# Optimization experiments

Hardware: AMD Instinct MI355X
Metric: run time of the kernel (lower is better)

## Reference

```python
import jax, jax.numpy as jnp
import numpy as np

LN_EPS = 1e-12
BIG = 1e30
BAND = 15  # end index may be at most 15 tokens after start


def output_layer(x, w1, b1, g, b, w2, b2):
    # Linear -> ReLU -> LayerNorm -> Linear (dropout is identity at eval)
    h = jax.nn.relu(x @ w1 + b1)
    mu = jnp.mean(h, axis=-1, keepdims=True)
    var = jnp.mean(jnp.square(h - mu), axis=-1, keepdims=True)
    h = (h - mu) * jax.lax.rsqrt(var + LN_EPS) * g + b
    return h @ w2 + b2


def setup_inputs() -> dict:
    key = jax.random.key(0)
    ks = jax.random.split(key, 8)
    B, S, D = 8, 4096, 1024
    H2 = 2 * D
    inp = {
        "context_input": jax.random.normal(ks[0], (B, S, D), jnp.float32),
        "context_mask": jnp.ones((B, S), jnp.float32),
    }
    def head(k1, k2, n_ans):
        return (
            0.02 * jax.random.normal(k1, (D, H2), jnp.float32),
            jnp.zeros((H2,), jnp.float32),
            jnp.ones((H2,), jnp.float32),
            jnp.zeros((H2,), jnp.float32),
            0.02 * jax.random.normal(k2, (H2, n_ans), jnp.float32),
            jnp.zeros((n_ans,), jnp.float32),
        )
    for name, k1, k2, n_ans in [("start", ks[1], ks[2], 1), ("end", ks[3], ks[4], 1), ("type", ks[5], ks[6], 4)]:
        w1, b1, g, b, w2, b2 = head(k1, k2, n_ans)
        inp[f"{name}_w1"] = w1; inp[f"{name}_b1"] = b1
        inp[f"{name}_g"] = g; inp[f"{name}_b"] = b
        inp[f"{name}_w2"] = w2; inp[f"{name}_b2"] = b2
    return inp


def reference(context_input, context_mask,
              start_w1, start_b1, start_g, start_b, start_w2, start_b2,
              end_w1, end_b1, end_g, end_b, end_w2, end_b2,
              type_w1, type_b1, type_g, type_b, type_w2, type_b2):
    S = context_input.shape[1]
    start_pred = output_layer(context_input, start_w1, start_b1, start_g, start_b, start_w2, start_b2)[..., 0] \
        - BIG * (1.0 - context_mask)  # [B,S]
    end_pred = output_layer(context_input, end_w1, end_b1, end_g, end_b, end_w2, end_b2)[..., 0] \
        - BIG * (1.0 - context_mask)  # [B,S]
    type_pred = output_layer(context_input[:, 0, :], type_w1, type_b1, type_g, type_b, type_w2, type_b2)  # [B,4]

    # outer[b,i,j] = start[b,i] + end[b,j], masked to band 0 <= j-i <= 15
    outer = start_pred[:, :, None] + end_pred[:, None, :]  # [B,S,S]
    i = jnp.arange(S)[:, None]
    j = jnp.arange(S)[None, :]
    band = ((j >= i) & (j <= i + BAND)).astype(outer.dtype)  # [S,S]
    outer = outer - BIG * (1.0 - band)[None]

    yp1 = jnp.argmax(jnp.max(outer, axis=2), axis=1)  # best start index [B]
    yp2 = jnp.argmax(jnp.max(outer, axis=1), axis=1)  # best end index [B]
    return start_pred, end_pred, type_pred, yp1, yp2
```

## Files before the change

kernel.cpp:

```cpp
#include <hip/hip_runtime.h>

typedef _Float16 f16x8 __attribute__((ext_vector_type(8)));
typedef float f32x4 __attribute__((ext_vector_type(4)));

#define BIGF 1e30f
#define M_TOT 32768
#define H2 2048

#define WS_XH 0u
#define WS_WT 67108864u
#define WS_BVEC 75497472u
#define WS_GW2 75513856u
#define WS_CONSTS 75530240u
#define WS_PART 75530496u
#define WS_TPART 100696320u

__global__ void k_convert_x(const float* __restrict__ x, _Float16* __restrict__ xh) {
  size_t i = ((size_t)blockIdx.x * 256 + threadIdx.x) * 8;
  float4 v0 = *(const float4*)(x + i);
  float4 v1 = *(const float4*)(x + i + 4);
  f16x8 h;
  h[0] = (_Float16)v0.x; h[1] = (_Float16)v0.y; h[2] = (_Float16)v0.z; h[3] = (_Float16)v0.w;
  h[4] = (_Float16)v1.x; h[5] = (_Float16)v1.y; h[6] = (_Float16)v1.z; h[7] = (_Float16)v1.w;
  *(f16x8*)(xh + i) = h;
}

__global__ void k_convert_w(const float* __restrict__ w_s, const float* __restrict__ w_e,
                            _Float16* __restrict__ wt) {
  __shared__ float tile[64][65];
  const float* w = blockIdx.z ? w_e : w_s;
  int n0 = blockIdx.x * 64, k0 = blockIdx.y * 64;
  int tx = threadIdx.x & 63, ty = threadIdx.x >> 6;
#pragma unroll
  for (int i = ty; i < 64; i += 4) tile[i][tx] = w[(size_t)(k0 + i) * H2 + n0 + tx];
  __syncthreads();
#pragma unroll
  for (int i = ty; i < 64; i += 4) {
    wt[((size_t)(blockIdx.z * H2 + n0 + i)) * 1024 + k0 + tx] = (_Float16)tile[tx][i];
  }
}

__global__ void k_prep(const float* __restrict__ s_b1, const float* __restrict__ s_g,
                       const float* __restrict__ s_w2, const float* __restrict__ s_b,
                       const float* __restrict__ s_b2, const float* __restrict__ e_b1,
                       const float* __restrict__ e_g, const float* __restrict__ e_w2,
                       const float* __restrict__ e_b, const float* __restrict__ e_b2,
                       float* __restrict__ bvec, float* __restrict__ gw2,
                       float* __restrict__ consts) {
  int blk = blockIdx.x;
  if (blk < 16) {
    int i = blk * 256 + threadIdx.x;
    int head = i >> 11, j = i & (H2 - 1);
    bvec[i] = head ? e_b1[j] : s_b1[j];
    gw2[i] = head ? e_g[j] * e_w2[j] : s_g[j] * s_w2[j];
  } else {
    int h = blk - 16;
    const float* g = h ? e_g : s_g;
    const float* b = h ? e_b : s_b;
    const float* w2 = h ? e_w2 : s_w2;
    const float* b2 = h ? e_b2 : s_b2;
    float c1 = 0.f, c2 = 0.f;
    for (int j = threadIdx.x; j < H2; j += 256) {
      float w = w2[j];
      c1 += g[j] * w;
      c2 += b[j] * w;
    }
    for (int m = 1; m < 64; m <<= 1) { c1 += __shfl_xor(c1, m); c2 += __shfl_xor(c2, m); }
    __shared__ float r1[4], r2[4];
    int wid = threadIdx.x >> 6;
    if ((threadIdx.x & 63) == 0) { r1[wid] = c1; r2[wid] = c2; }
    __syncthreads();
    if (threadIdx.x == 0) {
      consts[h * 2 + 0] = r1[0] + r1[1] + r1[2] + r1[3];
      consts[h * 2 + 1] = r2[0] + r2[1] + r2[2] + r2[3] + b2[0];
    }
  }
}

#define BUF 65536u
#define STA(q, tile, bufo)                                                              \
  __builtin_amdgcn_global_load_lds(                                                     \
      (const __attribute__((address_space(1))) unsigned int*)(srcA + (size_t)(q) * 131072 + (size_t)(tile) * 128), \
      (__attribute__((address_space(3))) unsigned int*)(lds + (bufo) + (q) * 8192 + t * 16), 16, 0, 0)
#define STB(q, tile, bufo)                                                              \
  __builtin_amdgcn_global_load_lds(                                                     \
      (const __attribute__((address_space(1))) unsigned int*)(srcB + (size_t)(q) * 131072 + (size_t)(tile) * 128), \
      (__attribute__((address_space(3))) unsigned int*)(lds + (bufo) + 32768u + (q) * 8192 + t * 16), 16, 0, 0)

#define READA(AF, mi0, BUFO)                                                            \
  AF[0][0] = *(const f16x8*)(lds + (BUFO) + arow + (mi0) * 2048 + low0);                \
  AF[0][1] = *(const f16x8*)(lds + (BUFO) + arow + (mi0) * 2048 + low1);                \
  AF[1][0] = *(const f16x8*)(lds + (BUFO) + arow + ((mi0) + 1) * 2048 + low0);          \
  AF[1][1] = *(const f16x8*)(lds + (BUFO) + arow + ((mi0) + 1) * 2048 + low1);

#define READB(BF, BUFO)                                                                 \
  _Pragma("unroll")                                                                     \
  for (int nj = 0; nj < 4; ++nj) {                                                      \
    BF[nj][0] = *(const f16x8*)(lds + (BUFO) + brow + nj * 2048 + low0);                \
    BF[nj][1] = *(const f16x8*)(lds + (BUFO) + brow + nj * 2048 + low1);                \
  }

#define MFMA2(m0, m1, AF, BF)                                                           \
  __builtin_amdgcn_s_setprio(1);                                                        \
  _Pragma("unroll")                                                                     \
  for (int nj = 0; nj < 4; ++nj) {                                                      \
    acc[m0][nj] = __builtin_amdgcn_mfma_f32_16x16x32_f16(AF[0][0], BF[nj][0], acc[m0][nj], 0, 0, 0); \
    acc[m1][nj] = __builtin_amdgcn_mfma_f32_16x16x32_f16(AF[1][0], BF[nj][0], acc[m1][nj], 0, 0, 0); \
  }                                                                                     \
  _Pragma("unroll")                                                                     \
  for (int nj = 0; nj < 4; ++nj) {                                                      \
    acc[m0][nj] = __builtin_amdgcn_mfma_f32_16x16x32_f16(AF[0][1], BF[nj][1], acc[m0][nj], 0, 0, 0); \
    acc[m1][nj] = __builtin_amdgcn_mfma_f32_16x16x32_f16(AF[1][1], BF[nj][1], acc[m1][nj], 0, 0, 0); \
  }                                                                                     \
  __builtin_amdgcn_s_setprio(0);

#define PHASE_TAIL                                                                      \
  __builtin_amdgcn_sched_barrier(0);                                                    \
  __builtin_amdgcn_s_barrier();                                                         \
  asm volatile("s_waitcnt lgkmcnt(0)" ::: "memory");                                    \
  __builtin_amdgcn_sched_barrier(0);

__global__ __launch_bounds__(512, 2) void k_gemm(const _Float16* __restrict__ Xh,
                                                 const _Float16* __restrict__ Wt,
                                                 const float* __restrict__ bvec,
                                                 const float* __restrict__ gw2,
                                                 float* __restrict__ partials) {
  __shared__ char lds[2 * BUF];
  const int bid = blockIdx.x;
  const int swzb = (bid & 7) * 256 + (bid >> 3);
  const int nb = swzb & 15;
  const int mb = swzb >> 4;
  const int t = threadIdx.x;
  const int lane = t & 63, wid = t >> 6;
  const int c15 = lane & 15, g4 = lane >> 4;
  const int wmg = wid >> 2;
  const int wn = (wid & 3) * 64;

  f32x4 acc[8][4];
#pragma unroll
  for (int i = 0; i < 8; ++i)
#pragma unroll
    for (int j = 0; j < 4; ++j) acc[i][j] = (f32x4){0.f, 0.f, 0.f, 0.f};

  const char* Abase = (const char*)(Xh + (size_t)mb * 256 * 1024);
  const char* Bbase = (const char*)(Wt + (size_t)nb * 256 * 1024);
  const int rowl = t >> 3;
  const int swz = ((t & 7) * 16) ^ ((rowl & 7) << 4);
  const char* srcA = Abase + (size_t)rowl * 2048 + swz;
  const char* srcB = Bbase + (size_t)rowl * 2048 + swz;

  const int xorv = (c15 & 7) << 4;
  const int low0 = (g4 * 16) ^ xorv;
  const int low1 = (64 + g4 * 16) ^ xorv;
  const int arow = (wmg * 128 + c15) * 128;
  const int brow = 32768 + (wn + c15) * 128;

  STA(0, 0, 0); STA(1, 0, 0); STA(2, 0, 0); STA(3, 0, 0);
  STB(0, 0, 0); STB(1, 0, 0); STB(2, 0, 0); STB(3, 0, 0);
  STB(0, 1, BUF); STB(1, 1, BUF); STB(2, 1, BUF); STB(3, 1, BUF);
  STA(0, 1, BUF); STA(2, 1, BUF);
  asm volatile("s_waitcnt vmcnt(6)" ::: "memory");
  __builtin_amdgcn_s_barrier();
  __builtin_amdgcn_sched_barrier(0);

  f16x8 af[2][2], bf[4][2];

#pragma unroll
  for (int g = 0; g < 16; ++g) {
    const unsigned OB = (unsigned)(g & 1) * BUF;
    const unsigned ON = OB ^ BUF;
    READB(bf, OB);
    READA(af, 0, OB);
    if (g < 15) { STA(1, g + 1, ON); STA(3, g + 1, ON); }
    PHASE_TAIL
    MFMA2(0, 1, af, bf);
    READA(af, 2, OB);
    if (g < 14) { STB(0, g + 2, OB); STB(1, g + 2, OB); }
    PHASE_TAIL
    MFMA2(2, 3, af, bf);
    READA(af, 4, OB);
    if (g < 14) { STB(2, g + 2, OB); STB(3, g + 2, OB); }
    PHASE_TAIL
    MFMA2(4, 5, af, bf);
    READA(af, 6, OB);
    if (g < 14) { STA(0, g + 2, OB); STA(2, g + 2, OB); }
    PHASE_TAIL
    MFMA2(6, 7, af, bf);
    if (g < 14) asm volatile("s_waitcnt vmcnt(6)" ::: "memory");
    else        asm volatile("s_waitcnt vmcnt(0)" ::: "memory");
    __builtin_amdgcn_s_barrier();
  }

  float bv[4], gv[4];
#pragma unroll
  for (int nj = 0; nj < 4; ++nj) {
    int col = nb * 256 + wn + nj * 16 + c15;
    bv[nj] = bvec[col];
    gv[nj] = gw2[col];
  }
  const int slice = nb * 4 + (wid & 3);
#pragma unroll
  for (int mi = 0; mi < 8; ++mi) {
#pragma unroll
    for (int r = 0; r < 4; ++r) {
      float s1 = 0.f, s2 = 0.f, s3 = 0.f;
#pragma unroll
      for (int nj = 0; nj < 4; ++nj) {
        float v = acc[mi][nj][r] + bv[nj];
        v = fmaxf(v, 0.f);
        s1 += v;
        s2 += v * v;
        s3 += v * gv[nj];
      }
#pragma unroll
      for (int m = 1; m < 16; m <<= 1) {
        s1 += __shfl_xor(s1, m);
        s2 += __shfl_xor(s2, m);
        s3 += __shfl_xor(s3, m);
      }
      if (c15 == 0) {
        int rowg = mb * 256 + wmg * 128 + mi * 16 + g4 * 4 + r;
        partials[((size_t)(slice * 3 + 0)) * M_TOT + rowg] = s1;
        partials[((size_t)(slice * 3 + 1)) * M_TOT + rowg] = s2;
        partials[((size_t)(slice * 3 + 2)) * M_TOT + rowg] = s3;
      }
    }
  }
}

__global__ void k_reduce(const float* __restrict__ partials, const float* __restrict__ consts,
                         const float* __restrict__ mask, float* __restrict__ out) {
  int m = blockIdx.x * 256 + threadIdx.x;
  float s1 = 0.f, s2 = 0.f, s3 = 0.f, e1 = 0.f, e2 = 0.f, e3 = 0.f;
  for (int nb2 = 0; nb2 < 32; ++nb2) {
    s1 += partials[((size_t)(nb2 * 3 + 0)) * M_TOT + m];
    s2 += partials[((size_t)(nb2 * 3 + 1)) * M_TOT + m];
    s3 += partials[((size_t)(nb2 * 3 + 2)) * M_TOT + m];
  }
  for (int nb2 = 32; nb2 < 64; ++nb2) {
    e1 += partials[((size_t)(nb2 * 3 + 0)) * M_TOT + m];
    e2 += partials[((size_t)(nb2 * 3 + 1)) * M_TOT + m];
    e3 += partials[((size_t)(nb2 * 3 + 2)) * M_TOT + m];
  }
  const float H = (float)H2;
  float mu = s1 / H;
  float var = fmaxf(s2 / H - mu * mu, 0.f);
  float rs = 1.f / sqrtf(var + 1e-12f);
  float score_s = rs * (s3 - mu * consts[0]) + consts[1];
  mu = e1 / H;
  var = fmaxf(e2 / H - mu * mu, 0.f);
  rs = 1.f / sqrtf(var + 1e-12f);
  float score_e = rs * (e3 - mu * consts[2]) + consts[3];
  float mk = BIGF * (1.f - mask[m]);
  out[m] = score_s - mk;
  out[M_TOT + m] = score_e - mk;
}

__global__ void k_type_partial(const float* __restrict__ X, const float* __restrict__ w1,
                               const float* __restrict__ b1, const float* __restrict__ g,
                               const float* __restrict__ w2, float* __restrict__ tpart) {
  __shared__ float xs[1024];
  int cb = blockIdx.x, tok = blockIdx.y, t = threadIdx.x;
  const float* xp = X + (size_t)tok * 4096 * 1024;
  for (int i = t; i < 1024; i += 256) xs[i] = xp[i];
  __syncthreads();
  int j = cb * 256 + t;
  float dot = 0.f;
  for (int k = 0; k < 1024; ++k) dot += xs[k] * w1[(size_t)k * H2 + j];
  float h = fmaxf(dot + b1[j], 0.f);
  float gj = g[j];
  float s[6];
  s[0] = h;
  s[1] = h * h;
#pragma unroll
  for (int c = 0; c < 4; ++c) s[2 + c] = h * gj * w2[j * 4 + c];
  for (int m = 1; m < 64; m <<= 1)
#pragma unroll
    for (int q = 0; q < 6; ++q) s[q] += __shfl_xor(s[q], m);
  __shared__ float red[4][6];
  int wid = t >> 6;
  if ((t & 63) == 0)
#pragma unroll
    for (int q = 0; q < 6; ++q) red[wid][q] = s[q];
  __syncthreads();
  if (t == 0)
#pragma unroll
    for (int q = 0; q < 6; ++q)
      tpart[(tok * 8 + cb) * 6 + q] = red[0][q] + red[1][q] + red[2][q] + red[3][q];
}

__global__ void k_type_final(const float* __restrict__ tpart, const float* __restrict__ g,
                             const float* __restrict__ bb, const float* __restrict__ w2,
                             const float* __restrict__ b2, float* __restrict__ out) {
  int t = threadIdx.x;
  float c1[4] = {0.f, 0.f, 0.f, 0.f}, c2[4] = {0.f, 0.f, 0.f, 0.f};
  for (int j = t; j < H2; j += 256) {
    float gj = g[j], bj = bb[j];
#pragma unroll
    for (int c = 0; c < 4; ++c) {
      float w = w2[j * 4 + c];
      c1[c] += gj * w;
      c2[c] += bj * w;
    }
  }
  for (int m = 1; m < 64; m <<= 1)
#pragma unroll
    for (int c = 0; c < 4; ++c) { c1[c] += __shfl_xor(c1[c], m); c2[c] += __shfl_xor(c2[c], m); }
  __shared__ float rC1[4][4], rC2[4][4];
  int wid = t >> 6;
  if ((t & 63) == 0)
#pragma unroll
    for (int c = 0; c < 4; ++c) { rC1[wid][c] = c1[c]; rC2[wid][c] = c2[c]; }
  __syncthreads();
  __shared__ float sC1[4], sC2[4];
  if (t < 4) {
    sC1[t] = rC1[0][t] + rC1[1][t] + rC1[2][t] + rC1[3][t];
    sC2[t] = rC2[0][t] + rC2[1][t] + rC2[2][t] + rC2[3][t];
  }
  __syncthreads();
  if (t < 32) {
    int tok = t >> 2, c = t & 3;
    float s1 = 0.f, s2 = 0.f, s3 = 0.f;
    for (int cb = 0; cb < 8; ++cb) {
      s1 += tpart[(tok * 8 + cb) * 6 + 0];
      s2 += tpart[(tok * 8 + cb) * 6 + 1];
      s3 += tpart[(tok * 8 + cb) * 6 + 2 + c];
    }
    float mu = s1 / (float)H2;
    float var = fmaxf(s2 / (float)H2 - mu * mu, 0.f);
    float rs = 1.f / sqrtf(var + 1e-12f);
    out[65536 + tok * 4 + c] = rs * (s3 - mu * sC1[c]) + sC2[c] + b2[c];
  }
}

__global__ void k_band(const float* __restrict__ preds, float* __restrict__ out) {
  __shared__ float ss[4096], se[4096];
  int b = blockIdx.x, t = threadIdx.x;
  for (int i = t; i < 4096; i += 256) {
    ss[i] = preds[(size_t)b * 4096 + i];
    se[i] = preds[M_TOT + (size_t)b * 4096 + i];
  }
  __syncthreads();
  float bv1 = -3.0e38f, bv2 = -3.0e38f;
  int bi1 = 0x7fffffff, bi2 = 0x7fffffff;
  for (int i = t; i < 4096; i += 256) {
    float m1 = -3.0e38f;
    int jmax = i + 15 < 4095 ? i + 15 : 4095;
    for (int j = i; j <= jmax; ++j) m1 = fmaxf(m1, se[j]);
    float v1 = ss[i] + m1;
    if (v1 > bv1 || (v1 == bv1 && i < bi1)) { bv1 = v1; bi1 = i; }
    float m2 = -3.0e38f;
    int imin = i - 15 > 0 ? i - 15 : 0;
    for (int j = imin; j <= i; ++j) m2 = fmaxf(m2, ss[j]);
    float v2 = se[i] + m2;
    if (v2 > bv2 || (v2 == bv2 && i < bi2)) { bv2 = v2; bi2 = i; }
  }
  for (int m = 1; m < 64; m <<= 1) {
    float ov = __shfl_xor(bv1, m);
    int oi = __shfl_xor(bi1, m);
    if (ov > bv1 || (ov == bv1 && oi < bi1)) { bv1 = ov; bi1 = oi; }
    ov = __shfl_xor(bv2, m);
    oi = __shfl_xor(bi2, m);
    if (ov > bv2 || (ov == bv2 && oi < bi2)) { bv2 = ov; bi2 = oi; }
  }
  __shared__ float rv[2][4];
  __shared__ int ri[2][4];
  int wid = t >> 6;
  if ((t & 63) == 0) { rv[0][wid] = bv1; ri[0][wid] = bi1; rv[1][wid] = bv2; ri[1][wid] = bi2; }
  __syncthreads();
  if (t == 0) {
    float v = rv[0][0];
    int ix = ri[0][0];
    for (int w = 1; w < 4; ++w)
      if (rv[0][w] > v || (rv[0][w] == v && ri[0][w] < ix)) { v = rv[0][w]; ix = ri[0][w]; }
    out[65568 + b] = (float)ix;
    v = rv[1][0];
    ix = ri[1][0];
    for (int w = 1; w < 4; ++w)
      if (rv[1][w] > v || (rv[1][w] == v && ri[1][w] < ix)) { v = rv[1][w]; ix = ri[1][w]; }
    out[65576 + b] = (float)ix;
  }
}

extern "C" void kernel_launch(void* const* d_in, const int* in_sizes, int n_in, void* d_out,
                              int out_size, void* d_ws, size_t ws_size, hipStream_t stream) {
  const float* X = (const float*)d_in[0];
  const float* mask = (const float*)d_in[1];
  const float* s_w1 = (const float*)d_in[2];
  const float* s_b1 = (const float*)d_in[3];
  const float* s_g = (const float*)d_in[4];
  const float* s_b = (const float*)d_in[5];
  const float* s_w2 = (const float*)d_in[6];
  const float* s_b2 = (const float*)d_in[7];
  const float* e_w1 = (const float*)d_in[8];
  const float* e_b1 = (const float*)d_in[9];
  const float* e_g = (const float*)d_in[10];
  const float* e_b = (const float*)d_in[11];
  const float* e_w2 = (const float*)d_in[12];
  const float* e_b2 = (const float*)d_in[13];
  const float* t_w1 = (const float*)d_in[14];
  const float* t_b1 = (const float*)d_in[15];
  const float* t_g = (const float*)d_in[16];
  const float* t_b = (const float*)d_in[17];
  const float* t_w2 = (const float*)d_in[18];
  const float* t_b2 = (const float*)d_in[19];

  char* ws = (char*)d_ws;
  _Float16* Xh = (_Float16*)(ws + WS_XH);
  _Float16* Wt = (_Float16*)(ws + WS_WT);
  float* bvec = (float*)(ws + WS_BVEC);
  float* gw2 = (float*)(ws + WS_GW2);
  float* consts = (float*)(ws + WS_CONSTS);
  float* partials = (float*)(ws + WS_PART);
  float* tpart = (float*)(ws + WS_TPART);
  float* out = (float*)d_out;

  k_convert_x<<<16384, 256, 0, stream>>>(X, Xh);
  k_convert_w<<<dim3(32, 16, 2), 256, 0, stream>>>(s_w1, e_w1, Wt);
  k_prep<<<18, 256, 0, stream>>>(s_b1, s_g, s_w2, s_b, s_b2, e_b1, e_g, e_w2, e_b, e_b2,
                                 bvec, gw2, consts);
  k_gemm<<<2048, 512, 0, stream>>>(Xh, Wt, bvec, gw2, partials);
  k_reduce<<<128, 256, 0, stream>>>(partials, consts, mask, out);
  k_type_partial<<<dim3(8, 8), 256, 0, stream>>>(X, t_w1, t_b1, t_g, t_w2, tpart);
  k_type_final<<<1, 256, 0, stream>>>(tpart, t_g, t_b, t_w2, t_b2, out);
  k_band<<<8, 256, 0, stream>>>(out, out);
}
```

Baseline: 422.9 us.

## Load B fragments directly from global into registers, stage only A in LDS

The GEMM kernel stops staging the weight (B) tile through LDS. Each lane now loads its B fragments straight from global memory into double-buffered registers one k-step ahead, and only the activation (A) tile goes through LDS via global_load_lds. This halves LDS usage and removes the B LDS reads and the per-phase barriers. The costs are uncoalesced per-lane 16-byte global loads for B, more registers, and a full vmcnt(0) wait each k-iteration, which leaves less overlap between loads and compute.

```diff
diff --git a/kernel.cpp b/kernel.cpp
--- a/kernel.cpp
+++ b/kernel.cpp
@@ -77,55 +77,58 @@
   }
 }
 
-#define BUF 65536u
-#define STA(q, tile, bufo)                                                              \
-  __builtin_amdgcn_global_load_lds(                                                     \
-      (const __attribute__((address_space(1))) unsigned int*)(srcA + (size_t)(q) * 131072 + (size_t)(tile) * 128), \
-      (__attribute__((address_space(3))) unsigned int*)(lds + (bufo) + (q) * 8192 + t * 16), 16, 0, 0)
-#define STB(q, tile, bufo)                                                              \
-  __builtin_amdgcn_global_load_lds(                                                     \
-      (const __attribute__((address_space(1))) unsigned int*)(srcB + (size_t)(q) * 131072 + (size_t)(tile) * 128), \
-      (__attribute__((address_space(3))) unsigned int*)(lds + (bufo) + 32768u + (q) * 8192 + t * 16), 16, 0, 0)
-
-#define READA(AF, mi0, BUFO)                                                            \
-  AF[0][0] = *(const f16x8*)(lds + (BUFO) + arow + (mi0) * 2048 + low0);                \
-  AF[0][1] = *(const f16x8*)(lds + (BUFO) + arow + (mi0) * 2048 + low1);                \
-  AF[1][0] = *(const f16x8*)(lds + (BUFO) + arow + ((mi0) + 1) * 2048 + low0);          \
-  AF[1][1] = *(const f16x8*)(lds + (BUFO) + arow + ((mi0) + 1) * 2048 + low1);
-
-#define READB(BF, BUFO)                                                                 \
+#define BUFA 32768u
+
+#define LDB(BF, gg)                                                                     \
   _Pragma("unroll")                                                                     \
   for (int nj = 0; nj < 4; ++nj) {                                                      \
-    BF[nj][0] = *(const f16x8*)(lds + (BUFO) + brow + nj * 2048 + low0);                \
-    BF[nj][1] = *(const f16x8*)(lds + (BUFO) + brow + nj * 2048 + low1);                \
-  }
-
-#define MFMA2(m0, m1, AF, BF)                                                           \
-  __builtin_amdgcn_s_setprio(1);                                                        \
+    BF[nj][0] = *(const f16x8*)(Bcol[nj] + (gg) * 128);                                 \
+    BF[nj][1] = *(const f16x8*)(Bcol[nj] + (gg) * 128 + 64);                            \
+  }
+
+#define STAGE_A(gg)                                                                     \
   _Pragma("unroll")                                                                     \
-  for (int nj = 0; nj < 4; ++nj) {                                                      \
-    acc[m0][nj] = __builtin_amdgcn_mfma_f32_16x16x32_f16(AF[0][0], BF[nj][0], acc[m0][nj], 0, 0, 0); \
-    acc[m1][nj] = __builtin_amdgcn_mfma_f32_16x16x32_f16(AF[1][0], BF[nj][0], acc[m1][nj], 0, 0, 0); \
-  }                                                                                     \
-  _Pragma("unroll")                                                                     \
-  for (int nj = 0; nj < 4; ++nj) {                                                      \
-    acc[m0][nj] = __builtin_amdgcn_mfma_f32_16x16x32_f16(AF[0][1], BF[nj][1], acc[m0][nj], 0, 0, 0); \
-    acc[m1][nj] = __builtin_amdgcn_mfma_f32_16x16x32_f16(AF[1][1], BF[nj][1], acc[m1][nj], 0, 0, 0); \
-  }                                                                                     \
-  __builtin_amdgcn_s_setprio(0);
-
-#define PHASE_TAIL                                                                      \
-  __builtin_amdgcn_sched_barrier(0);                                                    \
-  __builtin_amdgcn_s_barrier();                                                         \
-  asm volatile("s_waitcnt lgkmcnt(0)" ::: "memory");                                    \
-  __builtin_amdgcn_sched_barrier(0);
+  for (int q = 0; q < 4; ++q)                                                           \
+    __builtin_amdgcn_global_load_lds(                                                   \
+        (const __attribute__((address_space(1))) unsigned int*)(srcA + (size_t)q * 131072 + (size_t)(gg) * 128), \
+        (__attribute__((address_space(3))) unsigned int*)(lds + (((gg) & 1) ? BUFA : 0u) + q * 8192 + t * 16), \
+        16, 0, 0);
+
+#define K_ITER(g, BFC, BFN)                                                             \
+  {                                                                                     \
+    asm volatile("s_waitcnt vmcnt(0)" ::: "memory");                                    \
+    __builtin_amdgcn_s_barrier();                                                       \
+    __builtin_amdgcn_sched_barrier(0);                                                  \
+    if ((g) < 15) { LDB(BFN, (g) + 1); STAGE_A((g) + 1); }                              \
+    __builtin_amdgcn_sched_barrier(0);                                                  \
+    const unsigned ob = ((g) & 1) ? BUFA : 0u;                                          \
+    _Pragma("unroll")                                                                   \
+    for (int p = 0; p < 4; ++p) {                                                       \
+      f16x8 a0k0 = *(const f16x8*)(lds + ob + arow + (2 * p) * 2048 + low0);            \
+      f16x8 a0k1 = *(const f16x8*)(lds + ob + arow + (2 * p) * 2048 + low1);            \
+      f16x8 a1k0 = *(const f16x8*)(lds + ob + arow + (2 * p + 1) * 2048 + low0);        \
+      f16x8 a1k1 = *(const f16x8*)(lds + ob + arow + (2 * p + 1) * 2048 + low1);        \
+      __builtin_amdgcn_s_setprio(1);                                                    \
+      _Pragma("unroll")                                                                 \
+      for (int nj = 0; nj < 4; ++nj) {                                                  \
+        acc[2 * p][nj] = __builtin_amdgcn_mfma_f32_16x16x32_f16(a0k0, BFC[nj][0], acc[2 * p][nj], 0, 0, 0); \
+        acc[2 * p + 1][nj] = __builtin_amdgcn_mfma_f32_16x16x32_f16(a1k0, BFC[nj][0], acc[2 * p + 1][nj], 0, 0, 0); \
+      }                                                                                 \
+      _Pragma("unroll")                                                                 \
+      for (int nj = 0; nj < 4; ++nj) {                                                  \
+        acc[2 * p][nj] = __builtin_amdgcn_mfma_f32_16x16x32_f16(a0k1, BFC[nj][1], acc[2 * p][nj], 0, 0, 0); \
+        acc[2 * p + 1][nj] = __builtin_amdgcn_mfma_f32_16x16x32_f16(a1k1, BFC[nj][1], acc[2 * p + 1][nj], 0, 0, 0); \
+      }                                                                                 \
+      __builtin_amdgcn_s_setprio(0);                                                    \
+    }                                                                                   \
+  }
 
 __global__ __launch_bounds__(512, 2) void k_gemm(const _Float16* __restrict__ Xh,
                                                  const _Float16* __restrict__ Wt,
                                                  const float* __restrict__ bvec,
                                                  const float* __restrict__ gw2,
                                                  float* __restrict__ partials) {
-  __shared__ char lds[2 * BUF];
+  __shared__ char lds[2 * BUFA];
   const int bid = blockIdx.x;
   const int swzb = (bid & 7) * 256 + (bid >> 3);
   const int nb = swzb & 15;
@@ -143,52 +146,28 @@
     for (int j = 0; j < 4; ++j) acc[i][j] = (f32x4){0.f, 0.f, 0.f, 0.f};
 
   const char* Abase = (const char*)(Xh + (size_t)mb * 256 * 1024);
-  const char* Bbase = (const char*)(Wt + (size_t)nb * 256 * 1024);
   const int rowl = t >> 3;
   const int swz = ((t & 7) * 16) ^ ((rowl & 7) << 4);
   const char* srcA = Abase + (size_t)rowl * 2048 + swz;
-  const char* srcB = Bbase + (size_t)rowl * 2048 + swz;
+
+  const char* Bcol[4];
+#pragma unroll
+  for (int nj = 0; nj < 4; ++nj)
+    Bcol[nj] = (const char*)Wt + (size_t)(nb * 256 + wn + nj * 16 + c15) * 2048 + g4 * 16;
 
   const int xorv = (c15 & 7) << 4;
   const int low0 = (g4 * 16) ^ xorv;
   const int low1 = (64 + g4 * 16) ^ xorv;
   const int arow = (wmg * 128 + c15) * 128;
-  const int brow = 32768 + (wn + c15) * 128;
-
-  STA(0, 0, 0); STA(1, 0, 0); STA(2, 0, 0); STA(3, 0, 0);
-  STB(0, 0, 0); STB(1, 0, 0); STB(2, 0, 0); STB(3, 0, 0);
-  STB(0, 1, BUF); STB(1, 1, BUF); STB(2, 1, BUF); STB(3, 1, BUF);
-  STA(0, 1, BUF); STA(2, 1, BUF);
-  asm volatile("s_waitcnt vmcnt(6)" ::: "memory");
-  __builtin_amdgcn_s_barrier();
-  __builtin_amdgcn_sched_barrier(0);
-
-  f16x8 af[2][2], bf[4][2];
-
-#pragma unroll
-  for (int g = 0; g < 16; ++g) {
-    const unsigned OB = (unsigned)(g & 1) * BUF;
-    const unsigned ON = OB ^ BUF;
-    READB(bf, OB);
-    READA(af, 0, OB);
-    if (g < 15) { STA(1, g + 1, ON); STA(3, g + 1, ON); }
-    PHASE_TAIL
-    MFMA2(0, 1, af, bf);
-    READA(af, 2, OB);
-    if (g < 14) { STB(0, g + 2, OB); STB(1, g + 2, OB); }
-    PHASE_TAIL
-    MFMA2(2, 3, af, bf);
-    READA(af, 4, OB);
-    if (g < 14) { STB(2, g + 2, OB); STB(3, g + 2, OB); }
-    PHASE_TAIL
-    MFMA2(4, 5, af, bf);
-    READA(af, 6, OB);
-    if (g < 14) { STA(0, g + 2, OB); STA(2, g + 2, OB); }
-    PHASE_TAIL
-    MFMA2(6, 7, af, bf);
-    if (g < 14) asm volatile("s_waitcnt vmcnt(6)" ::: "memory");
-    else        asm volatile("s_waitcnt vmcnt(0)" ::: "memory");
-    __builtin_amdgcn_s_barrier();
+
+  f16x8 bfA[4][2], bfB[4][2];
+  LDB(bfA, 0)
+  STAGE_A(0)
+
+#pragma unroll
+  for (int gp = 0; gp < 8; ++gp) {
+    K_ITER(2 * gp, bfA, bfB)
+    K_ITER(2 * gp + 1, bfB, bfA)
   }
 
   float bv[4], gv[4];
```

Measured after the change: 547.6 us. +29.5%, slower.

## Reorder GEMM main loop to k-half-major phases with 4x4 MFMA blocks

Applied to the files above, without the earlier changes.

Restructures the double-buffered fp16 MFMA main loop. Each k-tile is now split into two k-halves, and each phase issues a 4x4 block of MFMAs over half the M rows, replacing the earlier 2x4 blocks that covered both k-halves. Fragment registers drop from twelve to eight f16x8 vectors. The prefetches for the next tile are regrouped so the A row groups already consumed and all of B are refilled together before the last phase. The intent is lower register pressure and a better balance of LDS reads against MFMA work, at the cost of extra workgroup barriers per iteration.

```diff
diff --git a/kernel.cpp b/kernel.cpp
--- a/kernel.cpp
+++ b/kernel.cpp
@@ -87,38 +87,40 @@
       (const __attribute__((address_space(1))) unsigned int*)(srcB + (size_t)(q) * 131072 + (size_t)(tile) * 128), \
       (__attribute__((address_space(3))) unsigned int*)(lds + (bufo) + 32768u + (q) * 8192 + t * 16), 16, 0, 0)
 
-#define READA(AF, mi0, BUFO)                                                            \
-  AF[0][0] = *(const f16x8*)(lds + (BUFO) + arow + (mi0) * 2048 + low0);                \
-  AF[0][1] = *(const f16x8*)(lds + (BUFO) + arow + (mi0) * 2048 + low1);                \
-  AF[1][0] = *(const f16x8*)(lds + (BUFO) + arow + ((mi0) + 1) * 2048 + low0);          \
-  AF[1][1] = *(const f16x8*)(lds + (BUFO) + arow + ((mi0) + 1) * 2048 + low1);
-
-#define READB(BF, BUFO)                                                                 \
+#define RD_B(kh)                                                                        \
   _Pragma("unroll")                                                                     \
-  for (int nj = 0; nj < 4; ++nj) {                                                      \
-    BF[nj][0] = *(const f16x8*)(lds + (BUFO) + brow + nj * 2048 + low0);                \
-    BF[nj][1] = *(const f16x8*)(lds + (BUFO) + brow + nj * 2048 + low1);                \
-  }
-
-#define MFMA2(m0, m1, AF, BF)                                                           \
-  __builtin_amdgcn_s_setprio(1);                                                        \
+  for (int nj = 0; nj < 4; ++nj)                                                        \
+    bf[nj] = *(const f16x8*)(lds + ob + 32768u +                                        \
+                             (unsigned)((wn + nj * 16 + c15) * 128) +                   \
+                             (unsigned)((((kh) * 64) + g4 * 16) ^ xorv));
+
+#define RD_A(mh, kh)                                                                    \
   _Pragma("unroll")                                                                     \
-  for (int nj = 0; nj < 4; ++nj) {                                                      \
-    acc[m0][nj] = __builtin_amdgcn_mfma_f32_16x16x32_f16(AF[0][0], BF[nj][0], acc[m0][nj], 0, 0, 0); \
-    acc[m1][nj] = __builtin_amdgcn_mfma_f32_16x16x32_f16(AF[1][0], BF[nj][0], acc[m1][nj], 0, 0, 0); \
-  }                                                                                     \
-  _Pragma("unroll")                                                                     \
-  for (int nj = 0; nj < 4; ++nj) {                                                      \
-    acc[m0][nj] = __builtin_amdgcn_mfma_f32_16x16x32_f16(AF[0][1], BF[nj][1], acc[m0][nj], 0, 0, 0); \
-    acc[m1][nj] = __builtin_amdgcn_mfma_f32_16x16x32_f16(AF[1][1], BF[nj][1], acc[m1][nj], 0, 0, 0); \
-  }                                                                                     \
-  __builtin_amdgcn_s_setprio(0);
-
-#define PHASE_TAIL                                                                      \
+  for (int i = 0; i < 4; ++i)                                                           \
+    af[i] = *(const f16x8*)(lds + ob +                                                  \
+                            (unsigned)((wmg * 128 + (mh) * 64 + i * 16 + c15) * 128) +  \
+                            (unsigned)((((kh) * 64) + g4 * 16) ^ xorv));
+
+#define PH_TAIL                                                                         \
   __builtin_amdgcn_sched_barrier(0);                                                    \
   __builtin_amdgcn_s_barrier();                                                         \
   asm volatile("s_waitcnt lgkmcnt(0)" ::: "memory");                                    \
   __builtin_amdgcn_sched_barrier(0);
+
+#define BAR2                                                                            \
+  __builtin_amdgcn_sched_barrier(0);                                                    \
+  __builtin_amdgcn_s_barrier();                                                         \
+  __builtin_amdgcn_sched_barrier(0);
+
+#define MF16(mh)                                                                        \
+  __builtin_amdgcn_s_setprio(1);                                                        \
+  _Pragma("unroll")                                                                     \
+  for (int i = 0; i < 4; ++i)                                                           \
+    _Pragma("unroll")                                                                   \
+    for (int nj = 0; nj < 4; ++nj)                                                      \
+      acc[(mh) * 4 + i][nj] =                                                           \
+          __builtin_amdgcn_mfma_f32_16x16x32_f16(af[i], bf[nj], acc[(mh) * 4 + i][nj], 0, 0, 0); \
+  __builtin_amdgcn_s_setprio(0);
 
 __global__ __launch_bounds__(512, 2) void k_gemm(const _Float16* __restrict__ Xh,
                                                  const _Float16* __restrict__ Wt,
@@ -150,10 +152,6 @@
   const char* srcB = Bbase + (size_t)rowl * 2048 + swz;
 
   const int xorv = (c15 & 7) << 4;
-  const int low0 = (g4 * 16) ^ xorv;
-  const int low1 = (64 + g4 * 16) ^ xorv;
-  const int arow = (wmg * 128 + c15) * 128;
-  const int brow = 32768 + (wn + c15) * 128;
 
   STA(0, 0, 0); STA(1, 0, 0); STA(2, 0, 0); STA(3, 0, 0);
   STB(0, 0, 0); STB(1, 0, 0); STB(2, 0, 0); STB(3, 0, 0);
@@ -163,32 +161,41 @@
   __builtin_amdgcn_s_barrier();
   __builtin_amdgcn_sched_barrier(0);
 
-  f16x8 af[2][2], bf[4][2];
+  f16x8 af[4], bf[4];
 
 #pragma unroll
   for (int g = 0; g < 16; ++g) {
-    const unsigned OB = (unsigned)(g & 1) * BUF;
-    const unsigned ON = OB ^ BUF;
-    READB(bf, OB);
-    READA(af, 0, OB);
-    if (g < 15) { STA(1, g + 1, ON); STA(3, g + 1, ON); }
-    PHASE_TAIL
-    MFMA2(0, 1, af, bf);
-    READA(af, 2, OB);
-    if (g < 14) { STB(0, g + 2, OB); STB(1, g + 2, OB); }
-    PHASE_TAIL
-    MFMA2(2, 3, af, bf);
-    READA(af, 4, OB);
-    if (g < 14) { STB(2, g + 2, OB); STB(3, g + 2, OB); }
-    PHASE_TAIL
-    MFMA2(4, 5, af, bf);
-    READA(af, 6, OB);
-    if (g < 14) { STA(0, g + 2, OB); STA(2, g + 2, OB); }
-    PHASE_TAIL
-    MFMA2(6, 7, af, bf);
-    if (g < 14) asm volatile("s_waitcnt vmcnt(6)" ::: "memory");
-    else        asm volatile("s_waitcnt vmcnt(0)" ::: "memory");
+    const unsigned ob = (unsigned)(g & 1) * BUF;
+    const unsigned on = ob ^ BUF;
+
+    if (g < 15) { STA(1, g + 1, on); STA(3, g + 1, on); }
+    RD_B(0); RD_A(0, 0);
+    PH_TAIL
+    MF16(0)
+    BAR2
+
+    RD_A(1, 0);
+    PH_TAIL
+    MF16(1)
+    BAR2
+
+    RD_B(1); RD_A(0, 1);
+    PH_TAIL
+    MF16(0)
+    BAR2
+
+    if (g < 14) {
+      STB(0, g + 2, ob); STB(1, g + 2, ob); STB(2, g + 2, ob); STB(3, g + 2, ob);
+      STA(0, g + 2, ob); STA(2, g + 2, ob);
+    }
+    RD_A(1, 1);
+    PH_TAIL
+    MF16(1)
+    __builtin_amdgcn_sched_barrier(0);
+    if (g < 14)       asm volatile("s_waitcnt vmcnt(6)" ::: "memory");
+    else if (g == 14) asm volatile("s_waitcnt vmcnt(0)" ::: "memory");
     __builtin_amdgcn_s_barrier();
+    __builtin_amdgcn_sched_barrier(0);
   }
 
   float bv[4], gv[4];
```

Result: no change. 430.5 us (+1.8%).
